# Performance work log

Measured on AMD Instinct MI355X. Metric: run time of the kernel, lower is better.

The kernel has to match this reference:

```python
import jax, jax.numpy as jnp
import numpy as np

TAU = 0.03        # self.tau
EPS = 0.65       # args.epsilon
EPS2 = 0.4       # args.epsilon2 (trimap)
LOGIT_T = 0.07    # logits temperature


def _l2norm(x, axis):
    # torch F.normalize: x / max(||x||, 1e-12)
    n = jnp.sqrt(jnp.sum(x * x, axis=axis, keepdims=True))
    return x / jnp.maximum(n, 1e-12)


def setup_inputs() -> dict:
    key = jax.random.key(0)
    k1, k2 = jax.random.split(key)
    img = jax.random.normal(k1, (256, 512, 14, 14), dtype=jnp.float32)
    aud = jax.random.normal(k2, (256, 512), dtype=jnp.float32)
    return {"img": img, "aud": aud}


def reference(img, aud):
    # img: [B, C, H, W] backbone vision features; aud: [B, C] pooled audio features
    B = img.shape[0]
    img = _l2norm(img, axis=1)
    aud = _l2norm(aud, axis=1)

    # A: paired audio-visual correlation map [B, 1, H, W]
    A = jnp.einsum('nchw,nc->nhw', img, aud)[:, None]
    # A0: full cross-pair correlation maps [B, B, H, W] (n = image idx, m = audio idx)
    A0 = jnp.einsum('nchw,mc->nmhw', img, aud)
    # AdaptiveMaxPool2d((1,1)) -> max over spatial dims -> [B, B]
    A0_ref = jnp.max(A0, axis=(2, 3))

    Pos = jax.nn.sigmoid((A - EPS) / TAU)           # [B, 1, H, W]
    Pos2 = jax.nn.sigmoid((A - EPS2) / TAU)         # trimap branch
    Neg = 1.0 - Pos2
    Pos_all = jax.nn.sigmoid((A0 - EPS) / TAU)      # [B, B, H, W]

    mask = 1.0 - 100.0 * jnp.eye(B, dtype=img.dtype)
    # gated weighted-mean pooling over spatial dims
    sim = (Pos_all * A0).sum(axis=(2, 3)) / Pos_all.sum(axis=(2, 3)) * mask   # [B, B]
    sim1 = (Pos * A).sum(axis=(2, 3)) / Pos.sum(axis=(2, 3))                  # [B, 1]
    sim2 = (Neg * A).sum(axis=(2, 3)) / Neg.sum(axis=(2, 3))                  # [B, 1]

    logits = jnp.concatenate((sim1, sim, sim2), axis=1) / LOGIT_T             # [B, B+2]
    return (A, logits, Pos, Neg, A0_ref)
```

## Files before the change

### kernel.cpp

```cpp
#include <hip/hip_runtime.h>
#include <math.h>

typedef _Float16 half8 __attribute__((ext_vector_type(8)));
typedef float f32x4 __attribute__((ext_vector_type(4)));

#define RLT (1.0f/0.07f)


__device__ __forceinline__ void gll16(const void* g, void* l) {
    __builtin_amdgcn_global_load_lds(
        (const __attribute__((address_space(1))) void*)g,
        (__attribute__((address_space(3))) void*)l, 16, 0, 0);
}

__global__ __launch_bounds__(256) void prep_aud_pk(const float* __restrict__ aud,
                                                   _Float16* __restrict__ aud_pk) {
    int m = blockIdx.x, t = threadIdx.x;
    float a0 = aud[m * 512 + t];
    float a1 = aud[m * 512 + 256 + t];
    float s = a0 * a0 + a1 * a1;
    #pragma unroll
    for (int off = 32; off; off >>= 1) s += __shfl_down(s, off, 64);
    __shared__ float wsum[4];
    __shared__ float rns;
    if ((t & 63) == 0) wsum[t >> 6] = s;
    __syncthreads();
    if (t == 0) rns = 1.0f / fmaxf(sqrtf(wsum[0] + wsum[1] + wsum[2] + wsum[3]), 1e-12f);
    __syncthreads();
    float rn = rns;
    int c0 = t, c1 = t + 256;
    aud_pk[(c0 >> 3) * 2048 + m * 8 + (c0 & 7)] = (_Float16)(a0 * rn);
    aud_pk[(c1 >> 3) * 2048 + m * 8 + (c1 & 7)] = (_Float16)(a1 * rn);
}

__global__ __launch_bounds__(512, 2) void av_one(const float* __restrict__ img,
                                                 const _Float16* __restrict__ aud_pk,
                                                 float* __restrict__ out) {
    const int n = blockIdx.x;
    const int tid = threadIdx.x;
    const int w = tid >> 6, l = tid & 63;
    const int q = w & 3;
    const int hh = w >> 2;
    const int HT = hh ? 6 : 7;
    const int kk = l >> 4, lm = l & 15;

    __shared__ _Float16 __align__(16) Abuf[2][4][208][8];
    __shared__ _Float16 __align__(16) Bbuf[2][4][256][8];
    __shared__ float nrm_parts[2][196];
    __shared__ float rnorm_s[208];
    __shared__ float red_max[2][256], red_sw[2][256], red_swa[2][256];
    __shared__ float diag_parts[2][4][4];

    if (tid < 96) {
        int b = tid / 48, rem = tid % 48, kg = rem / 12, row = 196 + rem % 12;
        *(float4*)&Abuf[b][kg][row][0] = make_float4(0.f, 0.f, 0.f, 0.f);
    }

    const float* imgn = img + (size_t)n * (512 * 196);
    const bool act = tid < 392;
    const int p   = act ? tid / 196 : 0;
    const int hwl = act ? tid % 196 : 0;
    float nrm = 0.f;
    float av0[16], av1[16];

    #define STAGE_B(t, buf)                                                         \
        do {                                                                        \
            const _Float16* g0 = aud_pk + (((size_t)(t) * 1024 + tid) << 3);        \
            _Float16* l0 = &Bbuf[buf][0][0][0] + ((w * 64) << 3);                   \
            gll16(g0, l0);                                                          \
            gll16(g0 + 4096, l0 + 4096);                                            \
        } while (0)

    #define LOAD_A_TO(dst, t)                                                       \
        do {                                                                        \
            const float* src = imgn + ((size_t)(32 * (t) + p * 16)) * 196 + hwl;    \
            _Pragma("unroll")                                                       \
            for (int i = 0; i < 16; i++) dst[i] = src[i * 196];                     \
            asm volatile("" :: "v"(dst[0]), "v"(dst[1]), "v"(dst[2]), "v"(dst[3]),  \
                               "v"(dst[4]), "v"(dst[5]), "v"(dst[6]), "v"(dst[7])); \
            asm volatile("" :: "v"(dst[8]), "v"(dst[9]), "v"(dst[10]), "v"(dst[11]),\
                               "v"(dst[12]), "v"(dst[13]), "v"(dst[14]), "v"(dst[15])); \
        } while (0)

    #define STAGE_A_FROM(srcv, buf)                                                 \
        do {                                                                        \
            if (act) {                                                              \
                half8 h0, h1;                                                       \
                _Pragma("unroll")                                                   \
                for (int i = 0; i < 8; i++) {                                       \
                    h0[i] = (_Float16)srcv[i];                                      \
                    h1[i] = (_Float16)srcv[8 + i];                                  \
                    nrm += srcv[i] * srcv[i] + srcv[8 + i] * srcv[8 + i];           \
                }                                                                   \
                *(half8*)&Abuf[buf][2 * p][hwl][0]     = h0;                        \
                *(half8*)&Abuf[buf][2 * p + 1][hwl][0] = h1;                        \
            }                                                                       \
        } while (0)

    STAGE_B(0, 0);
    asm volatile("" ::: "memory");
    LOAD_A_TO(av0, 0);
    asm volatile("" ::: "memory");
    STAGE_A_FROM(av0, 0);
    LOAD_A_TO(av1, 1);
    asm volatile("s_waitcnt lgkmcnt(0)" ::: "memory");
    __builtin_amdgcn_s_barrier();
    __builtin_amdgcn_sched_barrier(0);

    f32x4 acc[7][4];
    #pragma unroll
    for (int ht = 0; ht < 7; ht++)
        #pragma unroll
        for (int mt = 0; mt < 4; mt++)
            acc[ht][mt] = (f32x4){0.f, 0.f, 0.f, 0.f};

    const int aoff = kk * 1664 + (hh * 112 + lm) * 8;
    const int boff = kk * 2048 + (q * 64 + lm) * 8;

    #define STEP(t, cur, loadSlot, stageSlot)                                       \
        do {                                                                        \
            const int nb_ = (cur) ^ 1;                                              \
            if ((t) <= 14) STAGE_B((t) + 1, nb_);                                   \
            asm volatile("" ::: "memory");                                          \
            if ((t) <= 13) LOAD_A_TO(loadSlot, (t) + 2);                            \
            asm volatile("" ::: "memory");                                          \
            {                                                                       \
                const _Float16* Ab = &Abuf[cur][0][0][0];                           \
                const _Float16* Bb = &Bbuf[cur][0][0][0];                           \
                half8 afrag[7];                                                     \
                _Pragma("unroll")                                                   \
                for (int ht = 0; ht < 7; ht++)                                      \
                    if (ht < HT) afrag[ht] = *(const half8*)(Ab + aoff + ht * 128); \
                __builtin_amdgcn_s_setprio(1);                                      \
                _Pragma("unroll")                                                   \
                for (int mt = 0; mt < 4; mt++) {                                    \
                    half8 bfrag = *(const half8*)(Bb + boff + mt * 128);            \
                    _Pragma("unroll")                                               \
                    for (int ht = 0; ht < 7; ht++)                                  \
                        if (ht < HT)                                                \
                            acc[ht][mt] = __builtin_amdgcn_mfma_f32_16x16x32_f16(   \
                                afrag[ht], bfrag, acc[ht][mt], 0, 0, 0);            \
                }                                                                   \
                __builtin_amdgcn_s_setprio(0);                                      \
            }                                                                       \
            __builtin_amdgcn_sched_barrier(0);                                      \
            if ((t) <= 14) STAGE_A_FROM(stageSlot, nb_);                            \
            if ((t) < 15) {                                                         \
                asm volatile("s_waitcnt lgkmcnt(0)" ::: "memory");                  \
                if ((t) <= 13) asm volatile("s_waitcnt vmcnt(16)" ::: "memory");    \
                else           asm volatile("s_waitcnt vmcnt(0)" ::: "memory");     \
                __builtin_amdgcn_s_barrier();                                       \
                __builtin_amdgcn_sched_barrier(0);                                  \
            }                                                                       \
        } while (0)

    #pragma unroll
    for (int tt = 0; tt < 16; tt += 2) {
        STEP(tt,     0, av0, av1);
        STEP(tt + 1, 1, av1, av0);
    }

    #undef STEP
    #undef STAGE_B
    #undef LOAD_A_TO
    #undef STAGE_A_FROM

    if (act) nrm_parts[p][hwl] = nrm;
    __syncthreads();
    if (tid < 208) {
        float v = 0.f;
        if (tid < 196)
            v = 1.0f / fmaxf(sqrtf(nrm_parts[0][tid] + nrm_parts[1][tid]), 1e-12f);
        rnorm_s[tid] = v;
    }
    __syncthreads();

    float mx[4], sw[4], swa[4];
    #pragma unroll
    for (int mt = 0; mt < 4; mt++) { mx[mt] = -1e30f; sw[mt] = 0.f; swa[mt] = 0.f; }
    float s1n = 0.f, s1d = 0.f, s2n = 0.f, s2d = 0.f;
    const int dmt = (n >> 4) & 3, dq = n >> 6, dl = n & 15;
    const bool isdiag = (q == dq) && (lm == dl);

    #pragma unroll
    for (int ht = 0; ht < 7; ht++) {
        if (ht < HT) {
            int rowb = hh * 112 + ht * 16 + (kk << 2);
            #pragma unroll
            for (int r = 0; r < 4; r++) {
                int hw = rowb + r;
                float rn = rnorm_s[hw];
                bool valid = hw < 196;
                #pragma unroll
                for (int mt = 0; mt < 4; mt++) {
                    float a0 = acc[ht][mt][r] * rn;
                    if (valid) {
                        float wg = 1.0f / (1.0f + __expf((0.65f - a0) * (1.0f / 0.03f)));
                        mx[mt]  = fmaxf(mx[mt], a0);
                        sw[mt] += wg;
                        swa[mt] += wg * a0;
                        if (isdiag && mt == dmt) {
                            out[n * 196 + hw] = a0;
                            out[116224 + n * 196 + hw] = wg;
                            float p2 = 1.0f / (1.0f + __expf((0.40f - a0) * (1.0f / 0.03f)));
                            float ng = 1.0f - p2;
                            out[166400 + n * 196 + hw] = ng;
                            s1n += wg * a0; s1d += wg;
                            s2n += ng * a0; s2d += ng;
                        }
                    }
                }
            }
        }
    }

    #pragma unroll
    for (int mt = 0; mt < 4; mt++) {
        float m1 = mx[mt], v1 = sw[mt], v2 = swa[mt];
        m1 = fmaxf(m1, __shfl_xor(m1, 16, 64)); v1 += __shfl_xor(v1, 16, 64); v2 += __shfl_xor(v2, 16, 64);
        m1 = fmaxf(m1, __shfl_xor(m1, 32, 64)); v1 += __shfl_xor(v1, 32, 64); v2 += __shfl_xor(v2, 32, 64);
        if (l < 16) {
            int m = q * 64 + mt * 16 + l;
            red_max[hh][m] = m1; red_sw[hh][m] = v1; red_swa[hh][m] = v2;
        }
    }
    if (isdiag) {
        diag_parts[hh][kk][0] = s1n;
        diag_parts[hh][kk][1] = s1d;
        diag_parts[hh][kk][2] = s2n;
        diag_parts[hh][kk][3] = s2d;
    }
    __syncthreads();

    if (tid < 256) {
        int m = tid;
        float mxv = fmaxf(red_max[0][m], red_max[1][m]);
        float num = red_swa[0][m] + red_swa[1][m];
        float den = red_sw[0][m] + red_sw[1][m];
        float sim = num / den;
        if (m == n) sim *= -99.0f;
        out[50176 + n * 258 + 1 + m] = sim * RLT;
        out[216576 + n * 256 + m] = mxv;
        if (m == n) {
            float t1n = 0.f, t1d = 0.f, t2n = 0.f, t2d = 0.f;
            #pragma unroll
            for (int h2 = 0; h2 < 2; h2++)
                #pragma unroll
                for (int g2 = 0; g2 < 4; g2++) {
                    t1n += diag_parts[h2][g2][0]; t1d += diag_parts[h2][g2][1];
                    t2n += diag_parts[h2][g2][2]; t2d += diag_parts[h2][g2][3];
                }
            out[50176 + n * 258]       = (t1n / t1d) * RLT;
            out[50176 + n * 258 + 257] = (t2n / t2d) * RLT;
        }
    }
}

extern "C" void kernel_launch(void* const* d_in, const int* in_sizes, int n_in,
                              void* d_out, int out_size, void* d_ws, size_t ws_size,
                              hipStream_t stream) {
    const float* img = (const float*)d_in[0];
    const float* aud = (const float*)d_in[1];
    float* out = (float*)d_out;
    _Float16* aud_pk = (_Float16*)d_ws;

    prep_aud_pk<<<256, 256, 0, stream>>>(aud, aud_pk);
    av_one<<<256, 512, 0, stream>>>(img, aud_pk, out);
}
```

Measured before the change: 50.08 us.

## Load audio fragments into registers and give each wave full spatial extent

The audio operand now goes straight from global memory into registers, double-buffered per step, instead of being staged through LDS with async global-to-LDS loads. The wave split changes from 4 audio quarters × 2 spatial halves to 8 waves of 32 audio columns, each covering all 13 spatial tiles. This drops the cross-wave shared-memory reduction and its extra barrier, and removes the LDS traffic for B. In exchange, every wave now reads all A fragments from LDS and fetches B from L2 itself. The hand-placed vmcnt waits and compiler fences are gone, so load overlap is left to the compiler.

```diff
diff --git a/kernel.cpp b/kernel.cpp
--- a/kernel.cpp
+++ b/kernel.cpp
@@ -6,12 +6,6 @@
 
 #define RLT (1.0f/0.07f)
 
-
-__device__ __forceinline__ void gll16(const void* g, void* l) {
-    __builtin_amdgcn_global_load_lds(
-        (const __attribute__((address_space(1))) void*)g,
-        (__attribute__((address_space(3))) void*)l, 16, 0, 0);
-}
 
 __global__ __launch_bounds__(256) void prep_aud_pk(const float* __restrict__ aud,
                                                    _Float16* __restrict__ aud_pk) {
@@ -33,23 +27,17 @@
     aud_pk[(c1 >> 3) * 2048 + m * 8 + (c1 & 7)] = (_Float16)(a1 * rn);
 }
 
-__global__ __launch_bounds__(512, 2) void av_one(const float* __restrict__ img,
-                                                 const _Float16* __restrict__ aud_pk,
-                                                 float* __restrict__ out) {
+__global__ __launch_bounds__(512, 2) void av_breg(const float* __restrict__ img,
+                                                  const _Float16* __restrict__ aud_pk,
+                                                  float* __restrict__ out) {
     const int n = blockIdx.x;
     const int tid = threadIdx.x;
     const int w = tid >> 6, l = tid & 63;
-    const int q = w & 3;
-    const int hh = w >> 2;
-    const int HT = hh ? 6 : 7;
     const int kk = l >> 4, lm = l & 15;
 
     __shared__ _Float16 __align__(16) Abuf[2][4][208][8];
-    __shared__ _Float16 __align__(16) Bbuf[2][4][256][8];
     __shared__ float nrm_parts[2][196];
     __shared__ float rnorm_s[208];
-    __shared__ float red_max[2][256], red_sw[2][256], red_swa[2][256];
-    __shared__ float diag_parts[2][4][4];
 
     if (tid < 96) {
         int b = tid / 48, rem = tid % 48, kg = rem / 12, row = 196 + rem % 12;
@@ -62,24 +50,24 @@
     const int hwl = act ? tid % 196 : 0;
     float nrm = 0.f;
     float av0[16], av1[16];
-
-    #define STAGE_B(t, buf)                                                         \
-        do {                                                                        \
-            const _Float16* g0 = aud_pk + (((size_t)(t) * 1024 + tid) << 3);        \
-            _Float16* l0 = &Bbuf[buf][0][0][0] + ((w * 64) << 3);                   \
-            gll16(g0, l0);                                                          \
-            gll16(g0 + 4096, l0 + 4096);                                            \
+    half8 b0[2], b1[2];
+
+    const _Float16* bbase = aud_pk + (size_t)kk * 2048 + (32 * w + lm) * 8;
+
+    #define LOAD_B(dst, t)                                                          \
+        do {                                                                        \
+            const _Float16* bp = bbase + (size_t)(t) * 8192;                        \
+            dst[0] = *(const half8*)(bp);                                           \
+            dst[1] = *(const half8*)(bp + 128);                                     \
         } while (0)
 
     #define LOAD_A_TO(dst, t)                                                       \
         do {                                                                        \
-            const float* src = imgn + ((size_t)(32 * (t) + p * 16)) * 196 + hwl;    \
-            _Pragma("unroll")                                                       \
-            for (int i = 0; i < 16; i++) dst[i] = src[i * 196];                     \
-            asm volatile("" :: "v"(dst[0]), "v"(dst[1]), "v"(dst[2]), "v"(dst[3]),  \
-                               "v"(dst[4]), "v"(dst[5]), "v"(dst[6]), "v"(dst[7])); \
-            asm volatile("" :: "v"(dst[8]), "v"(dst[9]), "v"(dst[10]), "v"(dst[11]),\
-                               "v"(dst[12]), "v"(dst[13]), "v"(dst[14]), "v"(dst[15])); \
+            if (act) {                                                              \
+                const float* src = imgn + ((size_t)(32 * (t) + p * 16)) * 196 + hwl;\
+                _Pragma("unroll")                                                   \
+                for (int i = 0; i < 16; i++) dst[i] = src[i * 196];                 \
+            }                                                                       \
         } while (0)
 
     #define STAGE_A_FROM(srcv, buf)                                                 \
@@ -97,49 +85,38 @@
             }                                                                       \
         } while (0)
 
-    STAGE_B(0, 0);
-    asm volatile("" ::: "memory");
     LOAD_A_TO(av0, 0);
-    asm volatile("" ::: "memory");
+    LOAD_B(b0, 0);
     STAGE_A_FROM(av0, 0);
     LOAD_A_TO(av1, 1);
     asm volatile("s_waitcnt lgkmcnt(0)" ::: "memory");
     __builtin_amdgcn_s_barrier();
     __builtin_amdgcn_sched_barrier(0);
 
-    f32x4 acc[7][4];
-    #pragma unroll
-    for (int ht = 0; ht < 7; ht++)
-        #pragma unroll
-        for (int mt = 0; mt < 4; mt++)
-            acc[ht][mt] = (f32x4){0.f, 0.f, 0.f, 0.f};
-
-    const int aoff = kk * 1664 + (hh * 112 + lm) * 8;
-    const int boff = kk * 2048 + (q * 64 + lm) * 8;
-
-    #define STEP(t, cur, loadSlot, stageSlot)                                       \
+    f32x4 acc[13][2];
+    #pragma unroll
+    for (int ht = 0; ht < 13; ht++) {
+        acc[ht][0] = (f32x4){0.f, 0.f, 0.f, 0.f};
+        acc[ht][1] = (f32x4){0.f, 0.f, 0.f, 0.f};
+    }
+
+    const int aoff = kk * 1664 + lm * 8;
+
+    #define STEP(t, cur, bcur, bnxt, loadSlot, stageSlot)                           \
         do {                                                                        \
             const int nb_ = (cur) ^ 1;                                              \
-            if ((t) <= 14) STAGE_B((t) + 1, nb_);                                   \
-            asm volatile("" ::: "memory");                                          \
+            if ((t) <= 14) LOAD_B(bnxt, (t) + 1);                                   \
             if ((t) <= 13) LOAD_A_TO(loadSlot, (t) + 2);                            \
-            asm volatile("" ::: "memory");                                          \
             {                                                                       \
                 const _Float16* Ab = &Abuf[cur][0][0][0];                           \
-                const _Float16* Bb = &Bbuf[cur][0][0][0];                           \
-                half8 afrag[7];                                                     \
-                _Pragma("unroll")                                                   \
-                for (int ht = 0; ht < 7; ht++)                                      \
-                    if (ht < HT) afrag[ht] = *(const half8*)(Ab + aoff + ht * 128); \
                 __builtin_amdgcn_s_setprio(1);                                      \
                 _Pragma("unroll")                                                   \
-                for (int mt = 0; mt < 4; mt++) {                                    \
-                    half8 bfrag = *(const half8*)(Bb + boff + mt * 128);            \
-                    _Pragma("unroll")                                               \
-                    for (int ht = 0; ht < 7; ht++)                                  \
-                        if (ht < HT)                                                \
-                            acc[ht][mt] = __builtin_amdgcn_mfma_f32_16x16x32_f16(   \
-                                afrag[ht], bfrag, acc[ht][mt], 0, 0, 0);            \
+                for (int ht = 0; ht < 13; ht++) {                                   \
+                    half8 af = *(const half8*)(Ab + aoff + ht * 128);               \
+                    acc[ht][0] = __builtin_amdgcn_mfma_f32_16x16x32_f16(            \
+                        af, bcur[0], acc[ht][0], 0, 0, 0);                          \
+                    acc[ht][1] = __builtin_amdgcn_mfma_f32_16x16x32_f16(            \
+                        af, bcur[1], acc[ht][1], 0, 0, 0);                          \
                 }                                                                   \
                 __builtin_amdgcn_s_setprio(0);                                      \
             }                                                                       \
@@ -147,8 +124,6 @@
             if ((t) <= 14) STAGE_A_FROM(stageSlot, nb_);                            \
             if ((t) < 15) {                                                         \
                 asm volatile("s_waitcnt lgkmcnt(0)" ::: "memory");                  \
-                if ((t) <= 13) asm volatile("s_waitcnt vmcnt(16)" ::: "memory");    \
-                else           asm volatile("s_waitcnt vmcnt(0)" ::: "memory");     \
                 __builtin_amdgcn_s_barrier();                                       \
                 __builtin_amdgcn_sched_barrier(0);                                  \
             }                                                                       \
@@ -156,12 +131,12 @@
 
     #pragma unroll
     for (int tt = 0; tt < 16; tt += 2) {
-        STEP(tt,     0, av0, av1);
-        STEP(tt + 1, 1, av1, av0);
+        STEP(tt,     0, b0, b1, av0, av1);
+        STEP(tt + 1, 1, b1, b0, av1, av0);
     }
 
     #undef STEP
-    #undef STAGE_B
+    #undef LOAD_B
     #undef LOAD_A_TO
     #undef STAGE_A_FROM
 
@@ -175,39 +150,37 @@
     }
     __syncthreads();
 
-    float mx[4], sw[4], swa[4];
-    #pragma unroll
-    for (int mt = 0; mt < 4; mt++) { mx[mt] = -1e30f; sw[mt] = 0.f; swa[mt] = 0.f; }
+    float mx[2], sw[2], swa[2];
+    #pragma unroll
+    for (int mt = 0; mt < 2; mt++) { mx[mt] = -1e30f; sw[mt] = 0.f; swa[mt] = 0.f; }
     float s1n = 0.f, s1d = 0.f, s2n = 0.f, s2d = 0.f;
-    const int dmt = (n >> 4) & 3, dq = n >> 6, dl = n & 15;
-    const bool isdiag = (q == dq) && (lm == dl);
-
-    #pragma unroll
-    for (int ht = 0; ht < 7; ht++) {
-        if (ht < HT) {
-            int rowb = hh * 112 + ht * 16 + (kk << 2);
+    const int dw = n >> 5, dmt = (n >> 4) & 1, dlm = n & 15;
+    const bool isdiag = (w == dw) && (lm == dlm);
+
+    #pragma unroll
+    for (int ht = 0; ht < 13; ht++) {
+        int rowb = ht * 16 + (kk << 2);
+        #pragma unroll
+        for (int r = 0; r < 4; r++) {
+            int hw = rowb + r;
+            float rn = rnorm_s[hw];
+            bool valid = hw < 196;
             #pragma unroll
-            for (int r = 0; r < 4; r++) {
-                int hw = rowb + r;
-                float rn = rnorm_s[hw];
-                bool valid = hw < 196;
-                #pragma unroll
-                for (int mt = 0; mt < 4; mt++) {
-                    float a0 = acc[ht][mt][r] * rn;
-                    if (valid) {
-                        float wg = 1.0f / (1.0f + __expf((0.65f - a0) * (1.0f / 0.03f)));
-                        mx[mt]  = fmaxf(mx[mt], a0);
-                        sw[mt] += wg;
-                        swa[mt] += wg * a0;
-                        if (isdiag && mt == dmt) {
-                            out[n * 196 + hw] = a0;
-                            out[116224 + n * 196 + hw] = wg;
-                            float p2 = 1.0f / (1.0f + __expf((0.40f - a0) * (1.0f / 0.03f)));
-                            float ng = 1.0f - p2;
-                            out[166400 + n * 196 + hw] = ng;
-                            s1n += wg * a0; s1d += wg;
-                            s2n += ng * a0; s2d += ng;
-                        }
+            for (int mt = 0; mt < 2; mt++) {
+                float a0 = acc[ht][mt][r] * rn;
+                if (valid) {
+                    float wg = 1.0f / (1.0f + __expf((0.65f - a0) * (1.0f / 0.03f)));
+                    mx[mt]  = fmaxf(mx[mt], a0);
+                    sw[mt] += wg;
+                    swa[mt] += wg * a0;
+                    if (isdiag && mt == dmt) {
+                        out[n * 196 + hw] = a0;
+                        out[116224 + n * 196 + hw] = wg;
+                        float p2 = 1.0f / (1.0f + __expf((0.40f - a0) * (1.0f / 0.03f)));
+                        float ng = 1.0f - p2;
+                        out[166400 + n * 196 + hw] = ng;
+                        s1n += wg * a0; s1d += wg;
+                        s2n += ng * a0; s2d += ng;
                     }
                 }
             }
@@ -215,43 +188,27 @@
     }
 
     #pragma unroll
-    for (int mt = 0; mt < 4; mt++) {
+    for (int mt = 0; mt < 2; mt++) {
         float m1 = mx[mt], v1 = sw[mt], v2 = swa[mt];
         m1 = fmaxf(m1, __shfl_xor(m1, 16, 64)); v1 += __shfl_xor(v1, 16, 64); v2 += __shfl_xor(v2, 16, 64);
         m1 = fmaxf(m1, __shfl_xor(m1, 32, 64)); v1 += __shfl_xor(v1, 32, 64); v2 += __shfl_xor(v2, 32, 64);
         if (l < 16) {
-            int m = q * 64 + mt * 16 + l;
-            red_max[hh][m] = m1; red_sw[hh][m] = v1; red_swa[hh][m] = v2;
+            int m = w * 32 + mt * 16 + l;
+            float sim = v2 / v1;
+            if (m == n) sim *= -99.0f;
+            out[50176 + n * 258 + 1 + m] = sim * RLT;
+            out[216576 + n * 256 + m] = m1;
         }
     }
-    if (isdiag) {
-        diag_parts[hh][kk][0] = s1n;
-        diag_parts[hh][kk][1] = s1d;
-        diag_parts[hh][kk][2] = s2n;
-        diag_parts[hh][kk][3] = s2d;
-    }
-    __syncthreads();
-
-    if (tid < 256) {
-        int m = tid;
-        float mxv = fmaxf(red_max[0][m], red_max[1][m]);
-        float num = red_swa[0][m] + red_swa[1][m];
-        float den = red_sw[0][m] + red_sw[1][m];
-        float sim = num / den;
-        if (m == n) sim *= -99.0f;
-        out[50176 + n * 258 + 1 + m] = sim * RLT;
-        out[216576 + n * 256 + m] = mxv;
-        if (m == n) {
-            float t1n = 0.f, t1d = 0.f, t2n = 0.f, t2d = 0.f;
-            #pragma unroll
-            for (int h2 = 0; h2 < 2; h2++)
-                #pragma unroll
-                for (int g2 = 0; g2 < 4; g2++) {
-                    t1n += diag_parts[h2][g2][0]; t1d += diag_parts[h2][g2][1];
-                    t2n += diag_parts[h2][g2][2]; t2d += diag_parts[h2][g2][3];
-                }
-            out[50176 + n * 258]       = (t1n / t1d) * RLT;
-            out[50176 + n * 258 + 257] = (t2n / t2d) * RLT;
+    {
+        float a = s1n, b = s1d, c = s2n, d = s2d;
+        a += __shfl_xor(a, 16, 64); b += __shfl_xor(b, 16, 64);
+        c += __shfl_xor(c, 16, 64); d += __shfl_xor(d, 16, 64);
+        a += __shfl_xor(a, 32, 64); b += __shfl_xor(b, 32, 64);
+        c += __shfl_xor(c, 32, 64); d += __shfl_xor(d, 32, 64);
+        if (isdiag && l < 16) {
+            out[50176 + n * 258]       = (a / b) * RLT;
+            out[50176 + n * 258 + 257] = (c / d) * RLT;
         }
     }
 }
@@ -265,5 +222,5 @@
     _Float16* aud_pk = (_Float16*)d_ws;
 
     prep_aud_pk<<<256, 256, 0, stream>>>(aud, aud_pk);
-    av_one<<<256, 512, 0, stream>>>(img, aud_pk, out);
+    av_breg<<<256, 512, 0, stream>>>(img, aud_pk, out);
 }
```

After: 55.79 us. 11.4% more time.
